# Kernel optimization log

Measured on AMD Instinct MI355X. Metric: run time of the kernel, lower is better.

## Reference

```python
import jax, jax.numpy as jnp
import numpy as np

E = 1024   # embed_size
H = 16     # num_heads
D = E // H # head_dim
B, S = 4, 2048

def setup_inputs() -> dict:
    key = jax.random.key(0)
    ks = jax.random.split(key, 11)
    scale = 1.0 / np.sqrt(E)
    inp = {
        "Q": jax.random.normal(ks[0], (B, S, E), jnp.float32),
        "K": jax.random.normal(ks[1], (B, S, E), jnp.float32),
        "V": jax.random.normal(ks[2], (B, S, E), jnp.float32),
        "Wq": jax.random.uniform(ks[3], (E, E), jnp.float32, -scale, scale),
        "bq": jax.random.uniform(ks[4], (E,), jnp.float32, -scale, scale),
        "Wk": jax.random.uniform(ks[5], (E, E), jnp.float32, -scale, scale),
        "bk": jax.random.uniform(ks[6], (E,), jnp.float32, -scale, scale),
        "Wv": jax.random.uniform(ks[7], (E, E), jnp.float32, -scale, scale),
        "bv": jax.random.uniform(ks[8], (E,), jnp.float32, -scale, scale),
        "Wo": jax.random.uniform(ks[9], (E, E), jnp.float32, -scale, scale),
        "bo": jax.random.uniform(ks[10], (E,), jnp.float32, -scale, scale),
    }
    return inp

def reference(Q, K, V, Wq, bq, Wk, bk, Wv, bv, Wo, bo):
    b, sq, _ = Q.shape
    sk = K.shape[1]
    # Linear projections (torch Linear: x @ W.T + b), split into heads -> (b, H, s, D)
    q = (Q @ Wq.T + bq).reshape(b, sq, H, D).transpose(0, 2, 1, 3)
    k = (K @ Wk.T + bk).reshape(b, sk, H, D).transpose(0, 2, 1, 3)
    v = (V @ Wv.T + bv).reshape(b, sk, H, D).transpose(0, 2, 1, 3)
    scores = jnp.einsum('bhqd,bhkd->bhqk', q, k) / jnp.sqrt(jnp.float32(D))
    attn = jax.nn.softmax(scores, axis=-1)
    out = jnp.einsum('bhqk,bhkd->bhqd', attn, v)  # (b, H, sq, D)
    concat = out.transpose(0, 2, 1, 3).reshape(b, sq, E)
    return concat @ Wo.T + bo
```

## Files before the change

### kernel.cpp

```cpp
#include <hip/hip_runtime.h>
#include <hip/hip_bf16.h>

typedef unsigned short u16;
typedef unsigned int u32;
typedef __bf16 bf16x8 __attribute__((ext_vector_type(8)));
typedef float f32x4 __attribute__((ext_vector_type(4)));
typedef float f32x16 __attribute__((ext_vector_type(16)));
typedef unsigned int u32x2 __attribute__((ext_vector_type(2)));

constexpr int E_ = 1024, H_ = 16, D_ = 64, B_ = 4, S_ = 2048;
constexpr int GM = B_ * S_;
constexpr int GN = E_;
constexpr int GK = E_;

__device__ __forceinline__ u16 f2bf(float f) {
  union { float f; u32 u; } v; v.f = f;
  u32 r = v.u + 0x7fffu + ((v.u >> 16) & 1u);
  return (u16)(r >> 16);
}

__device__ __forceinline__ bf16x8 ld_bf16x8(const u16* p) {
  return *reinterpret_cast<const bf16x8*>(p);
}

__device__ __forceinline__ f32x4 mfma16(bf16x8 a, bf16x8 b, f32x4 c) {
  return __builtin_amdgcn_mfma_f32_16x16x32_bf16(a, b, c, 0, 0, 0);
}
__device__ __forceinline__ f32x16 mfma32(bf16x8 a, bf16x8 b, f32x16 c) {
  return __builtin_amdgcn_mfma_f32_32x32x16_bf16(a, b, c, 0, 0, 0);
}

__device__ __forceinline__ u32 cvtpk(float lo, float hi) {
  u32 r;
  asm("v_cvt_pk_bf16_f32 %0, %1, %2" : "=v"(r) : "v"(lo), "v"(hi));
  return r;
}

__device__ __forceinline__ void pl32swap(u32& a, u32& b) {
#if __has_builtin(__builtin_amdgcn_permlane32_swap)
  u32x2 r = __builtin_amdgcn_permlane32_swap(a, b, false, false);
  a = r.x; b = r.y;
#else
  asm volatile("v_permlane32_swap_b32 %0, %1" : "+v"(a), "+v"(b));
#endif
}

__device__ __forceinline__ float fexp2(float x) {
#if __has_builtin(__builtin_amdgcn_exp2f)
  return __builtin_amdgcn_exp2f(x);
#else
  return exp2f(x);
#endif
}

#define GLOAD_LDS16(gp, lp)                                                       \
  __builtin_amdgcn_global_load_lds(                                               \
      (const __attribute__((address_space(1))) u32*)(const void*)(gp),            \
      (__attribute__((address_space(3))) u32*)(void*)(lp), 16, 0, 0)

__global__ __launch_bounds__(256) void cvt7(
    const float4* __restrict__ s0, const float4* __restrict__ s1,
    const float4* __restrict__ s2, const float4* __restrict__ s3,
    const float4* __restrict__ s4, const float4* __restrict__ s5,
    const float4* __restrict__ s6,
    ushort4* __restrict__ d0, ushort4* __restrict__ d1,
    ushort4* __restrict__ d2, ushort4* __restrict__ d3,
    ushort4* __restrict__ d4, ushort4* __restrict__ d5,
    ushort4* __restrict__ d6) {
  long i = (long)blockIdx.x * 256 + threadIdx.x;
  const float4* s; ushort4* d; long j;
  if (i < 2097152L)      { s = s0; d = d0; j = i; }
  else if (i < 4194304L) { s = s1; d = d1; j = i - 2097152L; }
  else if (i < 6291456L) { s = s2; d = d2; j = i - 4194304L; }
  else if (i < 6553600L) { s = s3; d = d3; j = i - 6291456L; }
  else if (i < 6815744L) { s = s4; d = d4; j = i - 6553600L; }
  else if (i < 7077888L) { s = s5; d = d5; j = i - 6815744L; }
  else                   { s = s6; d = d6; j = i - 7077888L; }
  float4 v = s[j];
  ushort4 o;
  o.x = f2bf(v.x); o.y = f2bf(v.y); o.z = f2bf(v.z); o.w = f2bf(v.w);
  d[j] = o;
}

template <int MODE>
__global__ __launch_bounds__(256, 2) void gemm_bt(
    const u16* __restrict__ A, const u16* __restrict__ Bw,
    const float* __restrict__ bias, void* __restrict__ Cout, float scale) {
  __shared__ u16 As[128 * 32];
  __shared__ u16 Bs[128 * 32];
  const int tid = threadIdx.x;
  const int lane = tid & 63, w = tid >> 6;
  const int lr = lane & 15, lg = lane >> 4;
  const int bid = blockIdx.x;
  const int flat = (bid & 7) * 64 + (bid >> 3);
  const int bm = flat >> 3, bn = flat & 7;
  const int wm = (w >> 1) * 64, wn = (w & 1) * 64;

  f32x4 acc[4][4] = {};

  const int byte0 = (w * 2 + 0) * 1024 + lane * 16;
  const int byte1 = (w * 2 + 1) * 1024 + lane * 16;
  const int r0 = byte0 >> 6, c0 = (byte0 & 63) >> 1;
  const int r1 = byte1 >> 6, c1 = (byte1 & 63) >> 1;
  const u16* Arow0 = A + (size_t)(bm * 128 + r0) * GK + c0;
  const u16* Arow1 = A + (size_t)(bm * 128 + r1) * GK + c1;
  const u16* Brow0 = Bw + (size_t)(bn * 128 + r0) * GK + c0;
  const u16* Brow1 = Bw + (size_t)(bn * 128 + r1) * GK + c1;
  u16* As0 = &As[(w * 2 + 0) * 512];
  u16* As1 = &As[(w * 2 + 1) * 512];
  u16* Bs0 = &Bs[(w * 2 + 0) * 512];
  u16* Bs1 = &Bs[(w * 2 + 1) * 512];

  for (int kt = 0; kt < GK / 32; ++kt) {
    const int ko = kt * 32;
    GLOAD_LDS16(Arow0 + ko, As0);
    GLOAD_LDS16(Arow1 + ko, As1);
    GLOAD_LDS16(Brow0 + ko, Bs0);
    GLOAD_LDS16(Brow1 + ko, Bs1);
    __syncthreads();
    bf16x8 af[4], bf_[4];
#pragma unroll
    for (int mi = 0; mi < 4; ++mi)
      af[mi] = ld_bf16x8(&As[(wm + mi * 16 + lr) * 32 + lg * 8]);
#pragma unroll
    for (int ni = 0; ni < 4; ++ni)
      bf_[ni] = ld_bf16x8(&Bs[(wn + ni * 16 + lr) * 32 + lg * 8]);
#pragma unroll
    for (int mi = 0; mi < 4; ++mi)
#pragma unroll
      for (int ni = 0; ni < 4; ++ni)
        acc[mi][ni] = mfma16(af[mi], bf_[ni], acc[mi][ni]);
    __syncthreads();
  }

#pragma unroll
  for (int mi = 0; mi < 4; ++mi)
#pragma unroll
    for (int ni = 0; ni < 4; ++ni) {
      const int n = bn * 128 + wn + ni * 16 + lr;
      const float bv = bias[n];
#pragma unroll
      for (int r = 0; r < 4; ++r) {
        const int m = bm * 128 + wm + mi * 16 + lg * 4 + r;
        const float vv = (acc[mi][ni][r] + bv) * scale;
        const int b = m >> 11, s = m & 2047, h = n >> 6, d = n & 63;
        if (MODE == 0) {
          ((u16*)Cout)[(((size_t)(b * 16 + h) * 2048 + s) * 64) + d] = f2bf(vv);
        } else if (MODE == 1) {
          const int bh = b * 16 + h;
          const int t = s >> 6, ks = (s >> 4) & 3, h2 = (s >> 3) & 1, j = s & 7;
          const int dt = d >> 5, lane2 = h2 * 32 + (d & 31);
          ((u16*)Cout)[(size_t)(bh * 32 + t) * 4096 + (dt * 4 + ks) * 512 +
                       lane2 * 8 + j] = f2bf(vv);
        } else {
          ((float*)Cout)[(size_t)m * 1024 + n] = vv;
        }
      }
    }
}

__global__ __launch_bounds__(256, 2) void attn6(
    const u16* __restrict__ q, const u16* __restrict__ k,
    const u16* __restrict__ VB, u16* __restrict__ concat) {
  __shared__ u16 KT[2][64 * 64];
  const int tid = threadIdx.x, lane = tid & 63, w = tid >> 6;
  const int l31 = lane & 31, hi = lane >> 5;
  const int bid = blockIdx.x;
  const int flat = (bid & 7) * 64 + (bid >> 3);
  const int bh = flat >> 3, qt = flat & 7;
  const u16* qbp = q + (size_t)bh * S_ * D_;
  const char* kbase = (const char*)(k + (size_t)bh * S_ * D_);
  const int q0 = qt * 256 + w * 64;

  bf16x8 qf[2][4];
#pragma unroll
  for (int qs = 0; qs < 2; ++qs)
#pragma unroll
    for (int kc = 0; kc < 4; ++kc)
      qf[qs][kc] =
          ld_bf16x8(&qbp[(size_t)(q0 + qs * 32 + l31) * 64 + kc * 16 + hi * 8]);

  f32x16 acc[2][2] = {};
  float l_[2] = {0.f, 0.f};

  const int srow = w * 8 + (lane >> 3);
  const int cswz = (((lane & 7) ^ (lane >> 3)) << 4);
  const char* gk0 = kbase + (size_t)srow * 128 + cswz;
  const char* gk1 = kbase + (size_t)(32 + srow) * 128 + cswz;

  int col4[4];
#pragma unroll
  for (int c = 0; c < 4; ++c)
    col4[c] = (((c * 32 + hi * 16) ^ ((lane & 7) << 4)) >> 1);
  const int rrow = l31 * 64;

  const u16* vbase = VB + (size_t)bh * 32 * 4096 + lane * 8;

#define STAGE(t, buf)                                                     \
  do {                                                                    \
    GLOAD_LDS16(gk0 + (size_t)(t) * 8192, &KT[buf][(0 * 4 + w) * 512]);   \
    GLOAD_LDS16(gk1 + (size_t)(t) * 8192, &KT[buf][(1 * 4 + w) * 512]);   \
  } while (0)

  STAGE(0, 0);
  asm volatile("s_waitcnt vmcnt(0)" ::: "memory");
  __syncthreads();

  for (int t = 0; t < S_ / 64; ++t) {
    const int cur = t & 1, nxt = cur ^ 1;
    if (t < S_ / 64 - 1) STAGE(t + 1, nxt);

    const u16* vb_t = vbase + (size_t)t * 4096;
    bf16x8 vt[2][4];
#pragma unroll
    for (int ks = 0; ks < 4; ++ks) {
      vt[0][ks] = ld_bf16x8(vb_t + ks * 512);
      vt[1][ks] = ld_bf16x8(vb_t + (4 + ks) * 512);
    }

    f32x16 sF[2][2] = {};
#pragma unroll
    for (int st = 0; st < 2; ++st)
#pragma unroll
      for (int kc = 0; kc < 4; ++kc) {
        bf16x8 kf = ld_bf16x8(&KT[cur][st * 2048 + rrow + col4[kc]]);
        sF[0][st] = mfma32(kf, qf[0][kc], sF[0][st]);
        sF[1][st] = mfma32(kf, qf[1][kc], sF[1][st]);
      }

#pragma unroll
    for (int qs = 0; qs < 2; ++qs) {
      float s0 = 0.f, s1 = 0.f, s2 = 0.f, s3 = 0.f;
#pragma unroll
      for (int st = 0; st < 2; ++st)
#pragma unroll
        for (int e = 0; e < 16; e += 4) {
          const float p0 = fexp2(sF[qs][st][e + 0]);
          const float p1 = fexp2(sF[qs][st][e + 1]);
          const float p2 = fexp2(sF[qs][st][e + 2]);
          const float p3 = fexp2(sF[qs][st][e + 3]);
          sF[qs][st][e + 0] = p0; sF[qs][st][e + 1] = p1;
          sF[qs][st][e + 2] = p2; sF[qs][st][e + 3] = p3;
          s0 += p0; s1 += p1; s2 += p2; s3 += p3;
        }
      l_[qs] += (s0 + s1) + (s2 + s3);

#pragma unroll
      for (int ks = 0; ks < 4; ++ks) {
        const int st = ks >> 1, b = (ks & 1) * 8;
        u32 w0 = cvtpk(sF[qs][st][b + 0], sF[qs][st][b + 1]);
        u32 w1 = cvtpk(sF[qs][st][b + 2], sF[qs][st][b + 3]);
        u32 w2 = cvtpk(sF[qs][st][b + 4], sF[qs][st][b + 5]);
        u32 w3 = cvtpk(sF[qs][st][b + 6], sF[qs][st][b + 7]);
        pl32swap(w0, w2);
        pl32swap(w1, w3);
        union { u32 u[4]; bf16x8 v; } pa;
        pa.u[0] = w0; pa.u[1] = w1; pa.u[2] = w2; pa.u[3] = w3;
        acc[qs][0] = mfma32(vt[0][ks], pa.v, acc[qs][0]);
        acc[qs][1] = mfma32(vt[1][ks], pa.v, acc[qs][1]);
      }
    }

    asm volatile("s_waitcnt vmcnt(0)" ::: "memory");
    __syncthreads();
  }
#undef STAGE

  const int b = bh >> 4, h = bh & 15;
#pragma unroll
  for (int qs = 0; qs < 2; ++qs) {
    u32 la = __builtin_bit_cast(u32, l_[qs]), lb = la;
    pl32swap(la, lb);
    const float lt =
        __builtin_bit_cast(float, la) + __builtin_bit_cast(float, lb);
    const float inv = 1.f / lt;
    const int s = q0 + qs * 32 + l31;
    u16* crow = concat + ((size_t)(b * 2048 + s)) * 1024 + h * 64;
#pragma unroll
    for (int dt = 0; dt < 2; ++dt)
#pragma unroll
      for (int g = 0; g < 4; ++g) {
        ushort4 o;
        o.x = f2bf(acc[qs][dt][g * 4 + 0] * inv);
        o.y = f2bf(acc[qs][dt][g * 4 + 1] * inv);
        o.z = f2bf(acc[qs][dt][g * 4 + 2] * inv);
        o.w = f2bf(acc[qs][dt][g * 4 + 3] * inv);
        *(ushort4*)&crow[dt * 32 + g * 8 + hi * 4] = o;
      }
  }
}

extern "C" void kernel_launch(void* const* d_in, const int* in_sizes, int n_in,
                              void* d_out, int out_size, void* d_ws,
                              size_t ws_size, hipStream_t stream) {
  const float* Qf = (const float*)d_in[0];
  const float* Kf = (const float*)d_in[1];
  const float* Vf = (const float*)d_in[2];
  const float* Wq = (const float*)d_in[3];
  const float* bq = (const float*)d_in[4];
  const float* Wk = (const float*)d_in[5];
  const float* bk = (const float*)d_in[6];
  const float* Wv = (const float*)d_in[7];
  const float* bv = (const float*)d_in[8];
  const float* Wo = (const float*)d_in[9];
  const float* bo = (const float*)d_in[10];

  char* ws = (char*)d_ws;
  u16* Xq = (u16*)(ws);
  u16* Xk = Xq + 8388608;
  u16* Xv = Xk + 8388608;
  u16* Wqb = (u16*)(ws + (size_t)3 * 16777216);
  u16* Wkb = Wqb + 1048576;
  u16* Wvb = Wkb + 1048576;
  u16* Wob = Wvb + 1048576;
  u16* qb = (u16*)(ws + (size_t)3 * 16777216 + 8388608);
  u16* kb = qb + (size_t)GM * GN;
  u16* VBb = kb + (size_t)GM * GN;
  u16* concat = Xq;

  cvt7<<<28672, 256, 0, stream>>>(
      (const float4*)Qf, (const float4*)Kf, (const float4*)Vf,
      (const float4*)Wq, (const float4*)Wk, (const float4*)Wv,
      (const float4*)Wo, (ushort4*)Xq, (ushort4*)Xk, (ushort4*)Xv,
      (ushort4*)Wqb, (ushort4*)Wkb, (ushort4*)Wvb, (ushort4*)Wob);

  gemm_bt<0><<<512, 256, 0, stream>>>(Xq, Wqb, bq, qb, 0.18033688011112042f);
  gemm_bt<0><<<512, 256, 0, stream>>>(Xk, Wkb, bk, kb, 1.0f);
  gemm_bt<1><<<512, 256, 0, stream>>>(Xv, Wvb, bv, VBb, 1.0f);

  attn6<<<512, 256, 0, stream>>>(qb, kb, VBb, concat);

  gemm_bt<2><<<512, 256, 0, stream>>>(concat, Wob, bo, (void*)d_out, 1.0f);
}
```

Measured before the change: 202.3 us.

## Double GEMM K-tile to 64 with XOR-swizzled shared memory layout

The projection GEMM kernel now stages a 64-wide K slice per iteration instead of 32, halving the number of barrier pairs and loop iterations. Global-to-LDS loads use an XOR swizzle on the 16-byte column chunk so that the fragment reads from shared memory avoid bank conflicts with the wider 128-byte rows. This doubles LDS use per block, to 32 KB, which may affect occupancy at two blocks per CU.

```diff
diff --git a/kernel.cpp b/kernel.cpp
--- a/kernel.cpp
+++ b/kernel.cpp
@@ -86,8 +86,8 @@
 __global__ __launch_bounds__(256, 2) void gemm_bt(
     const u16* __restrict__ A, const u16* __restrict__ Bw,
     const float* __restrict__ bias, void* __restrict__ Cout, float scale) {
-  __shared__ u16 As[128 * 32];
-  __shared__ u16 Bs[128 * 32];
+  __shared__ u16 As[128 * 64];
+  __shared__ u16 Bs[128 * 64];
   const int tid = threadIdx.x;
   const int lane = tid & 63, w = tid >> 6;
   const int lr = lane & 15, lg = lane >> 4;
@@ -98,38 +98,44 @@
 
   f32x4 acc[4][4] = {};
 
-  const int byte0 = (w * 2 + 0) * 1024 + lane * 16;
-  const int byte1 = (w * 2 + 1) * 1024 + lane * 16;
-  const int r0 = byte0 >> 6, c0 = (byte0 & 63) >> 1;
-  const int r1 = byte1 >> 6, c1 = (byte1 & 63) >> 1;
-  const u16* Arow0 = A + (size_t)(bm * 128 + r0) * GK + c0;
-  const u16* Arow1 = A + (size_t)(bm * 128 + r1) * GK + c1;
-  const u16* Brow0 = Bw + (size_t)(bn * 128 + r0) * GK + c0;
-  const u16* Brow1 = Bw + (size_t)(bn * 128 + r1) * GK + c1;
-  u16* As0 = &As[(w * 2 + 0) * 512];
-  u16* As1 = &As[(w * 2 + 1) * 512];
-  u16* Bs0 = &Bs[(w * 2 + 0) * 512];
-  u16* Bs1 = &Bs[(w * 2 + 1) * 512];
-
-  for (int kt = 0; kt < GK / 32; ++kt) {
-    const int ko = kt * 32;
-    GLOAD_LDS16(Arow0 + ko, As0);
-    GLOAD_LDS16(Arow1 + ko, As1);
-    GLOAD_LDS16(Brow0 + ko, Bs0);
-    GLOAD_LDS16(Brow1 + ko, Bs1);
+  const int srow = lane >> 3;
+  const int scol = ((lane & 7) ^ srow) << 3;
+  const u16* Arow[4];
+  const u16* Brow[4];
+#pragma unroll
+  for (int i = 0; i < 4; ++i) {
+    const int r = (w * 4 + i) * 8 + srow;
+    Arow[i] = A + (size_t)(bm * 128 + r) * GK + scol;
+    Brow[i] = Bw + (size_t)(bn * 128 + r) * GK + scol;
+  }
+
+  for (int kt = 0; kt < GK / 64; ++kt) {
+    const int ko = kt * 64;
+#pragma unroll
+    for (int i = 0; i < 4; ++i) {
+      GLOAD_LDS16(Arow[i] + ko, &As[(w * 4 + i) * 512]);
+      GLOAD_LDS16(Brow[i] + ko, &Bs[(w * 4 + i) * 512]);
+    }
     __syncthreads();
-    bf16x8 af[4], bf_[4];
-#pragma unroll
-    for (int mi = 0; mi < 4; ++mi)
-      af[mi] = ld_bf16x8(&As[(wm + mi * 16 + lr) * 32 + lg * 8]);
-#pragma unroll
-    for (int ni = 0; ni < 4; ++ni)
-      bf_[ni] = ld_bf16x8(&Bs[(wn + ni * 16 + lr) * 32 + lg * 8]);
-#pragma unroll
-    for (int mi = 0; mi < 4; ++mi)
-#pragma unroll
-      for (int ni = 0; ni < 4; ++ni)
-        acc[mi][ni] = mfma16(af[mi], bf_[ni], acc[mi][ni]);
+#pragma unroll
+    for (int kk = 0; kk < 2; ++kk) {
+      bf16x8 af[4], bf_[4];
+#pragma unroll
+      for (int mi = 0; mi < 4; ++mi) {
+        const int row = wm + mi * 16 + lr;
+        af[mi] = ld_bf16x8(&As[row * 64 + (((kk * 4 + lg) ^ (row & 7)) << 3)]);
+      }
+#pragma unroll
+      for (int ni = 0; ni < 4; ++ni) {
+        const int row = wn + ni * 16 + lr;
+        bf_[ni] = ld_bf16x8(&Bs[row * 64 + (((kk * 4 + lg) ^ (row & 7)) << 3)]);
+      }
+#pragma unroll
+      for (int mi = 0; mi < 4; ++mi)
+#pragma unroll
+        for (int ni = 0; ni < 4; ++ni)
+          acc[mi][ni] = mfma16(af[mi], bf_[ni], acc[mi][ni]);
+    }
     __syncthreads();
   }
 
```

Result: faster. 186.3 us, median of 2 (-7.9%).
